# Optimization experiments

Hardware: AMD Instinct MI355X
Metric: run time of the kernel (lower is better)

The kernel has to match this reference:

```python
import jax, jax.numpy as jnp
import numpy as np

B = 131072
NF, E = 9, 8
D0 = NF * E  # 72
H = 64       # expert hidden
O = 8        # expert output
T, SE, SH = 3, 3, 3
VOCAB = 160000

PARAM_SHAPES = {
    "emb_table": (VOCAB, E),
    "spec0_W1": (T, SE, D0, H), "spec0_b1": (T, SE, H),
    "spec0_W2": (T, SE, H, O),  "spec0_b2": (T, SE, O),
    "shar0_W1": (SH, D0, H),    "shar0_b1": (SH, H),
    "shar0_W2": (SH, H, O),     "shar0_b2": (SH, O),
    "gate0_W1": (T, D0, H),     "gate0_b1": (T, H),
    "gate0_W2": (T, H, O),      "gate0_b2": (T, O),
    "gate0_W3": (T, O, SE + SH),
    "sgate0_W1": (D0, H), "sgate0_b1": (H,),
    "sgate0_W2": (H, O),  "sgate0_b2": (O,),
    "sgate0_W3": (O, T * SE + SH),
    "spec1_W1": (T, SE, O, H), "spec1_b1": (T, SE, H),
    "spec1_W2": (T, SE, H, O), "spec1_b2": (T, SE, O),
    "shar1_W1": (SH, O, H),    "shar1_b1": (SH, H),
    "shar1_W2": (SH, H, O),    "shar1_b2": (SH, O),
    "gate1_W1": (T, O, H),     "gate1_b1": (T, H),
    "gate1_W2": (T, H, O),     "gate1_b2": (T, O),
    "gate1_W3": (T, O, SE + SH),
    "tower_W": (T, O, 1), "tower_b": (T, 1),
}


def setup_inputs() -> dict:
    key = jax.random.key(0)
    keys = jax.random.split(key, len(PARAM_SHAPES) + 1)
    inp = {n: jax.random.normal(k, s, jnp.float32) * 0.1
           for (n, s), k in zip(PARAM_SHAPES.items(), keys[:-1])}
    inp["cat_idx"] = jax.random.randint(keys[-1], (B, NF), 0, VOCAB, jnp.int32)
    return inp


def _cgc(task_x, shared_x, sW1, sb1, sW2, sb2, hW1, hb1, hW2, hb2,
         gW1, gb1, gW2, gb2, gW3, sgate=None):
    """One CGC level. task_x: [T,B,in], shared_x: [B,in]."""
    # task-specific experts, batched over (task, expert)
    h = jax.nn.relu(jnp.einsum('tbi,teih->tebh', task_x, sW1) + sb1[:, :, None, :])
    spec = jax.nn.relu(jnp.einsum('tebh,teho->tebo', h, sW2) + sb2[:, :, None, :])  # [T,SE,B,O]
    # shared experts, batched over expert
    hs = jax.nn.relu(jnp.einsum('bi,eih->ebh', shared_x, hW1) + hb1[:, None, :])
    shar = jax.nn.relu(jnp.einsum('ebh,eho->ebo', hs, hW2) + hb2[:, None, :])       # [SH,B,O]
    # per-task gates: MLP[64,8] relu -> linear(no bias) -> softmax over SE+SH experts
    g = jax.nn.relu(jnp.einsum('tbi,tih->tbh', task_x, gW1) + gb1[:, None, :])
    g = jax.nn.relu(jnp.einsum('tbh,tho->tbo', g, gW2) + gb2[:, None, :])
    gw = jax.nn.softmax(jnp.einsum('tbo,toe->tbe', g, gW3), axis=-1)                # [T,B,SE+SH]
    experts = jnp.concatenate(
        [spec, jnp.broadcast_to(shar[None], (spec.shape[0],) + shar.shape)], axis=1)  # [T,SE+SH,B,O]
    task_out = jnp.einsum('tebo,tbe->tbo', experts, gw)                             # [T,B,O]
    if sgate is None:
        return task_out, None
    sgW1, sgb1, sgW2, sgb2, sgW3 = sgate
    gs = jax.nn.relu(shared_x @ sgW1 + sgb1)
    gs = jax.nn.relu(gs @ sgW2 + sgb2)
    gws = jax.nn.softmax(gs @ sgW3, axis=-1)                                        # [B,T*SE+SH]
    all_e = jnp.concatenate([spec.reshape(T * SE, spec.shape[2], O), shar], axis=0)  # [T*SE+SH,B,O]
    shared_out = jnp.einsum('ebo,be->bo', all_e, gws)
    return task_out, shared_out


def _forward(cat_idx, p):
    x = p["emb_table"][cat_idx].reshape(cat_idx.shape[0], -1)  # [B, 72]
    task_x = jnp.broadcast_to(x[None], (T,) + x.shape)
    task_x, shared_x = _cgc(
        task_x, x,
        p["spec0_W1"], p["spec0_b1"], p["spec0_W2"], p["spec0_b2"],
        p["shar0_W1"], p["shar0_b1"], p["shar0_W2"], p["shar0_b2"],
        p["gate0_W1"], p["gate0_b1"], p["gate0_W2"], p["gate0_b2"], p["gate0_W3"],
        sgate=(p["sgate0_W1"], p["sgate0_b1"], p["sgate0_W2"], p["sgate0_b2"], p["sgate0_W3"]))
    task_x, _ = _cgc(
        task_x, shared_x,
        p["spec1_W1"], p["spec1_b1"], p["spec1_W2"], p["spec1_b2"],
        p["shar1_W1"], p["shar1_b1"], p["shar1_W2"], p["shar1_b2"],
        p["gate1_W1"], p["gate1_b1"], p["gate1_W2"], p["gate1_b2"], p["gate1_W3"],
        sgate=None)
    # 3 sigmoid towers -> stacked [T, B, 1] (== dict task_0..task_2 in original)
    out = jax.nn.sigmoid(jnp.einsum('tbo,tok->tbk', task_x, p["tower_W"]) + p["tower_b"][:, None, :])
    return out


def reference(cat_idx, emb_table, spec0_W1, spec0_b1, spec0_W2, spec0_b2,
              shar0_W1, shar0_b1, shar0_W2, shar0_b2,
              gate0_W1, gate0_b1, gate0_W2, gate0_b2, gate0_W3,
              sgate0_W1, sgate0_b1, sgate0_W2, sgate0_b2, sgate0_W3,
              spec1_W1, spec1_b1, spec1_W2, spec1_b2,
              shar1_W1, shar1_b1, shar1_W2, shar1_b2,
              gate1_W1, gate1_b1, gate1_W2, gate1_b2, gate1_W3,
              tower_W, tower_b):
    p = dict(locals())
    p.pop('cat_idx')
    return _forward(cat_idx, p)
```

## Files before the change

### kernel.cpp

```cpp
#include <hip/hip_runtime.h>


#define NT 256
#define EPB 64

typedef unsigned short u16;
typedef unsigned int u32;
typedef __fp16 hv2 __attribute__((ext_vector_type(2)));
typedef __fp16 half8 __attribute__((ext_vector_type(8)));
typedef __attribute__((ext_vector_type(4))) float floatx4;

__device__ __forceinline__ u32 pkh2(float a, float b){
  hv2 v = __builtin_amdgcn_cvt_pkrtz(a, b);
  u32 r; __builtin_memcpy(&r, &v, 4); return r;
}
__device__ __forceinline__ u16 f2h(float a){
  __fp16 h = (__fp16)a; u16 r; __builtin_memcpy(&r, &h, 2); return r;
}
__device__ __forceinline__ float h2f(u16 v){
  __fp16 h; __builtin_memcpy(&h, &v, 2); return (float)h;
}
__device__ __forceinline__ float dot2(u32 a, u32 b, float c){
  hv2 av, bv; __builtin_memcpy(&av, &a, 4); __builtin_memcpy(&bv, &b, 4);
  return __builtin_amdgcn_fdot2(av, bv, c, false);
}

__device__ __forceinline__ int pi2(int s){
  return (s & 3)*16 + (s >> 2);
}

#define W1F0 0
#define W2F0 49152
#define W1F1 57344
#define W2F1 72704
#define OFF_b1P0 80384
#define OFF_b2P0 81408
#define OFF_b1P1 81664
#define OFF_b2P1 82624
#define OFF_G0W3 82864
#define OFF_SG0W3 83008
#define OFF_G1W3 83104
#define OFF_TW   83248
#define OFF_Tb   83272
#define CVT_TOTAL 83275

struct PSrc { const float* p[33]; };

__global__ void cvt_kernel(PSrc S, u32* __restrict__ wsU, float* __restrict__ wsF){
  int i = blockIdx.x*256 + threadIdx.x;
  if (i >= CVT_TOTAL) return;
  if (i < 49152){
    int j2 = i & 3, l = (i>>2)&63, tt = (i>>8)&3;
    int rest = i >> 10; int s = rest % 3, u = rest / 3;
    int k0 = s*32 + (l>>4)*8 + 2*j2;
    int h  = tt*16 + (l&15);
    const float* src = (u<9)  ? S.p[0]  + (u*72)*64
                     : (u<12) ? S.p[4]  + ((u-9)*72)*64
                     : (u<15) ? S.p[8]  + ((u-12)*72)*64
                              : S.p[13];
    float lo = (k0   < 72) ? src[(k0  )*64 + h] : 0.f;
    float hi = (k0+1 < 72) ? src[(k0+1)*64 + h] : 0.f;
    wsU[i] = pkh2(lo, hi);
    return;
  }
  i -= 49152;
  if (i < 8192){
    int j2 = i & 3, l = (i>>2)&63, ks = (i>>8)&1, u = i>>9;
    int s0 = ks*32 + (l>>4)*8 + 2*j2;
    int n = l & 15;
    const float* src = (u<9)  ? S.p[2]  + u*512
                     : (u<12) ? S.p[6]  + (u-9)*512
                     : (u<15) ? S.p[10] + (u-12)*512
                              : S.p[15];
    float lo = (n<8) ? src[pi2((s0  )&63)*8 + n] : 0.f;
    float hi = (n<8) ? src[pi2((s0+1)&63)*8 + n] : 0.f;
    wsU[W2F0 + i] = pkh2(lo, hi);
    return;
  }
  i -= 8192;
  if (i < 15360){
    int j2 = i & 3, l = (i>>2)&63, tt = (i>>8)&3, u = i>>10;
    int k0 = (l>>4)*8 + 2*j2;
    int n = tt*16 + (l&15);
    const float* src = (u<9) ? S.p[18] + (u*8)*64
                     : (u<12) ? S.p[22] + ((u-9)*8)*64
                              : S.p[26] + ((u-12)*8)*64;
    float lo = (k0   < 8) ? src[(k0  )*64 + n] : 0.f;
    float hi = (k0+1 < 8) ? src[(k0+1)*64 + n] : 0.f;
    wsU[W1F1 + i] = pkh2(lo, hi);
    return;
  }
  i -= 15360;
  if (i < 7680){
    int j2 = i & 3, l = (i>>2)&63, ks = (i>>8)&1, u = i>>9;
    int s0 = ks*32 + (l>>4)*8 + 2*j2;
    int n = l & 15;
    const float* src = (u<9) ? S.p[20] + u*512
                     : (u<12) ? S.p[24] + (u-9)*512
                              : S.p[28] + (u-12)*512;
    float lo = (n<8) ? src[pi2((s0  )&63)*8 + n] : 0.f;
    float hi = (n<8) ? src[pi2((s0+1)&63)*8 + n] : 0.f;
    wsU[W2F1 + i] = pkh2(lo, hi);
    return;
  }
  i -= 7680;
  if (i < 1024){
    int u = i>>6, r = i&63, c16 = r>>2, t = r&3;
    const float* src = (u<9) ? S.p[1]+u*64 : (u<12) ? S.p[5]+(u-9)*64
                     : (u<15) ? S.p[9]+(u-12)*64 : S.p[14];
    wsF[OFF_b1P0 + i] = src[t*16 + c16];
    return;
  }
  i -= 1024;
  if (i < 256){
    int u = i>>4, n = i&15;
    const float* src = (u<9) ? S.p[3]+u*8 : (u<12) ? S.p[7]+(u-9)*8
                     : (u<15) ? S.p[11]+(u-12)*8 : S.p[16];
    wsF[OFF_b2P0 + i] = (n<8) ? src[n] : 0.f;
    return;
  }
  i -= 256;
  if (i < 960){
    int u = i>>6, r = i&63, c16 = r>>2, t = r&3;
    const float* src = (u<9) ? S.p[19]+u*64 : (u<12) ? S.p[23]+(u-9)*64
                               : S.p[27]+(u-12)*64;
    wsF[OFF_b1P1 + i] = src[t*16 + c16];
    return;
  }
  i -= 960;
  if (i < 240){
    int u = i>>4, n = i&15;
    const float* src = (u<9) ? S.p[21]+u*8 : (u<12) ? S.p[25]+(u-9)*8
                               : S.p[29]+(u-12)*8;
    wsF[OFF_b2P1 + i] = (n<8) ? src[n] : 0.f;
    return;
  }
  i -= 240;
  if (i < 144){ wsF[OFF_G0W3 + i] = S.p[12][i]; return; }
  i -= 144;
  if (i < 96){ wsF[OFF_SG0W3 + i] = S.p[17][i]; return; }
  i -= 96;
  if (i < 144){ wsF[OFF_G1W3 + i] = S.p[30][i]; return; }
  i -= 144;
  if (i < 24){ wsF[OFF_TW + i] = S.p[31][i]; return; }
  i -= 24;
  wsF[OFF_Tb + i] = S.p[32][i];
}

template<int N>
__device__ __forceinline__ void softmaxT(float (&v)[N]){
  float m = v[0];
  #pragma unroll
  for (int i=1;i<N;i++) m = fmaxf(m, v[i]);
  float s = 0.f;
  #pragma unroll
  for (int i=0;i<N;i++){ v[i] = __expf(v[i]-m); s += v[i]; }
  float inv = 1.f/s;
  #pragma unroll
  for (int i=0;i<N;i++) v[i] *= inv;
}

__global__ __launch_bounds__(NT, 4) void ple_kernel(
    const float* __restrict__ emb, const int* __restrict__ cat,
    const u32* __restrict__ wsU, const float* __restrict__ P,
    float* __restrict__ out, int Btot)
{
  __shared__ u32 S_[9984];
  u32* xsA = S_;
  u32* obT = S_ + 3328;
  u32* hbW = S_ + 7680;
  const int tid = threadIdx.x;
  const int e = tid & 63;
  const int su = __builtin_amdgcn_readfirstlane(tid >> 6);
  const int lane = tid & 63;
  const int q = lane >> 4;
  const int c16 = lane & 15;
  const int shw_e = ((e>>2)&1)*4;

  {
    const int eg = blockIdx.x*EPB + e;
    auto ldf = [&](int f){
      int idx = cat[eg*9 + f];
      const float* ep = emb + (long)idx*8;
      float4 a = *(const float4*)ep;
      float4 b = *(const float4*)(ep+4);
      uint4 w; w.x = pkh2(a.x,a.y); w.y = pkh2(a.z,a.w);
      w.z = pkh2(b.x,b.y); w.w = pkh2(b.z,b.w);
      *(uint4*)(xsA + e*52 + f*4) = w;
    };
    ldf(su); ldf(su+4);
    if (su == 0) ldf(8);
    *(uint4*)(xsA + e*52 + 36 + su*4) = (uint4){0,0,0,0};
  }
  __syncthreads();

  u16* obp = (u16*)obT;
  const int sh16_q = ((q&1) ? 8 : 0);

  {
    u32* hbU = hbW + su*576;
    #pragma unroll 1
    for (int k4 = 0; k4 < 4; k4++){
      const int u = su*4 + k4;
      half8 bf[3][4];
      #pragma unroll
      for (int s=0;s<3;s++)
        #pragma unroll
        for (int t=0;t<4;t++)
          bf[s][t] = *(const half8*)(wsU + W1F0 + (((u*3+s)*4+t)*64 + lane)*4);
      float4 bias4 = *(const float4*)(P + OFF_b1P0 + u*64 + c16*4);
      float bias[4] = {bias4.x, bias4.y, bias4.z, bias4.w};
      const float ob2 = P[OFF_b2P0 + u*16 + c16];
      half8 w2f[2];
      #pragma unroll
      for (int ks=0;ks<2;ks++)
        w2f[ks] = *(const half8*)(wsU + W2F0 + ((u*2+ks)*64 + lane)*4);

      #pragma unroll 1
      for (int m=0;m<4;m++){
        half8 af[3];
        #pragma unroll
        for (int s=0;s<3;s++)
          af[s] = *(const half8*)(xsA + (m*16 + c16)*52 + s*16 + q*4);
        floatx4 acc[4];
        #pragma unroll
        for (int t=0;t<4;t++) acc[t] = (floatx4){bias[t],bias[t],bias[t],bias[t]};
        #pragma unroll
        for (int s=0;s<3;s++)
          #pragma unroll
          for (int t=0;t<4;t++)
            acc[t] = __builtin_amdgcn_mfma_f32_16x16x32_f16(af[s], bf[s][t], acc[t], 0,0,0);
        #pragma unroll
        for (int r=0;r<4;r++){
          uint2 hw;
          hw.x = pkh2(fmaxf(acc[0][r],0.f), fmaxf(acc[1][r],0.f));
          hw.y = pkh2(fmaxf(acc[2][r],0.f), fmaxf(acc[3][r],0.f));
          *(uint2*)(hbU + (q*4+r)*36 + 2*c16) = hw;
        }
        floatx4 oc = (floatx4){ob2, ob2, ob2, ob2};
        #pragma unroll
        for (int ks=0;ks<2;ks++){
          half8 haf = *(const half8*)(hbU + c16*36 + ks*16 + q*4);
          oc = __builtin_amdgcn_mfma_f32_16x16x32_f16(haf, w2f[ks], oc, 0,0,0);
        }
        if (c16 < 8){
          #pragma unroll
          for (int r=0;r<4;r++)
            obp[(m*16 + q*4 + r)*136 + sh16_q + c16*16 + u] = f2h(fmaxf(oc[r], 0.f));
        }
      }
    }
  }
  __syncthreads();

  u32* l1in = xsA;
  *(uint4*)(l1in + e*36 + 16 + su*4) = (uint4){0,0,0,0};
  {
    float wv[12];
    {
      const int ug = (su<3) ? 12+su : 15;
      float g8[8];
      #pragma unroll
      for (int j=0;j<8;j++) g8[j] = h2f(obp[e*136 + 2*shw_e + j*16 + ug]);
      if (su < 3){
        float lg[6];
        #pragma unroll
        for (int m=0;m<6;m++){
          float s = 0.f;
          #pragma unroll
          for (int j=0;j<8;j++) s = fmaf(g8[j], P[OFF_G0W3 + su*48 + j*6 + m], s);
          lg[m] = s;
        }
        softmaxT<6>(lg);
        #pragma unroll
        for (int k=0;k<12;k++)
          wv[k] = (k<9) ? (((k/3)==su) ? lg[k%3] : 0.f) : lg[k-6];
      } else {
        float lw[12];
        #pragma unroll
        for (int m=0;m<12;m++){
          float s = 0.f;
          #pragma unroll
          for (int j=0;j<8;j++) s = fmaf(g8[j], P[OFF_SG0W3 + j*12 + m], s);
          lw[m] = s;
        }
        softmaxT<12>(lw);
        #pragma unroll
        for (int k=0;k<12;k++) wv[k] = lw[k];
      }
    }
    u32 wp[6];
    #pragma unroll
    for (int p=0;p<6;p++) wp[p] = pkh2(wv[2*p], wv[2*p+1]);
    float in8[8];
    #pragma unroll
    for (int n=0;n<8;n++){
      const u32* rowp = obT + e*68 + shw_e + n*8;
      uint4 A = *(const uint4*)rowp;
      uint2 Bv = *(const uint2*)(rowp + 4);
      float s = dot2(A.x, wp[0], 0.f);
      s = dot2(A.y, wp[1], s);
      s = dot2(A.z, wp[2], s);
      s = dot2(A.w, wp[3], s);
      s = dot2(Bv.x, wp[4], s);
      s = dot2(Bv.y, wp[5], s);
      in8[n] = s;
    }
    const int dst = (su<3) ? su*4 : 12;
    uint4 lw4; lw4.x = pkh2(in8[0],in8[1]); lw4.y = pkh2(in8[2],in8[3]);
    lw4.z = pkh2(in8[4],in8[5]); lw4.w = pkh2(in8[6],in8[7]);
    *(uint4*)(l1in + e*36 + dst) = lw4;
  }
  __syncthreads();

  {
    u32* hbU = hbW + su*576;
    #pragma unroll 1
    for (int k4=0;k4<4;k4++){
      const int u = su*4 + k4;
      if (u >= 15) break;
      const int base_u = (u<9) ? (u/3)*4 : ((u<12) ? 12 : (u-12)*4);
      const int aoff = (q==0) ? base_u : (16 + q*4);
      half8 bf1[4];
      #pragma unroll
      for (int t=0;t<4;t++)
        bf1[t] = *(const half8*)(wsU + W1F1 + ((u*4+t)*64 + lane)*4);
      float4 bias4 = *(const float4*)(P + OFF_b1P1 + u*64 + c16*4);
      float bias[4] = {bias4.x, bias4.y, bias4.z, bias4.w};
      const float ob2 = P[OFF_b2P1 + u*16 + c16];
      half8 w2f[2];
      #pragma unroll
      for (int ks=0;ks<2;ks++)
        w2f[ks] = *(const half8*)(wsU + W2F1 + ((u*2+ks)*64 + lane)*4);

      #pragma unroll 1
      for (int m=0;m<4;m++){
        half8 af = *(const half8*)(l1in + (m*16 + c16)*36 + aoff);
        floatx4 acc[4];
        #pragma unroll
        for (int t=0;t<4;t++) acc[t] = (floatx4){bias[t],bias[t],bias[t],bias[t]};
        #pragma unroll
        for (int t=0;t<4;t++)
          acc[t] = __builtin_amdgcn_mfma_f32_16x16x32_f16(af, bf1[t], acc[t], 0,0,0);
        #pragma unroll
        for (int r=0;r<4;r++){
          uint2 hw;
          hw.x = pkh2(fmaxf(acc[0][r],0.f), fmaxf(acc[1][r],0.f));
          hw.y = pkh2(fmaxf(acc[2][r],0.f), fmaxf(acc[3][r],0.f));
          *(uint2*)(hbU + (q*4+r)*36 + 2*c16) = hw;
        }
        floatx4 oc = (floatx4){ob2, ob2, ob2, ob2};
        #pragma unroll
        for (int ks=0;ks<2;ks++){
          half8 haf = *(const half8*)(hbU + c16*36 + ks*16 + q*4);
          oc = __builtin_amdgcn_mfma_f32_16x16x32_f16(haf, w2f[ks], oc, 0,0,0);
        }
        if (c16 < 8){
          #pragma unroll
          for (int r=0;r<4;r++)
            obp[(m*16 + q*4 + r)*136 + sh16_q + c16*16 + u] = f2h(fmaxf(oc[r], 0.f));
        }
      }
    }
  }
  __syncthreads();

  if (su < 3){
    const int t = su;
    float g8[8];
    #pragma unroll
    for (int j=0;j<8;j++) g8[j] = h2f(obp[e*136 + 2*shw_e + j*16 + 12+t]);
    float lg[6];
    #pragma unroll
    for (int m=0;m<6;m++){
      float s = 0.f;
      #pragma unroll
      for (int j=0;j<8;j++) s = fmaf(g8[j], P[OFF_G1W3 + t*48 + j*6 + m], s);
      lg[m] = s;
    }
    softmaxT<6>(lg);
    float wv[12];
    #pragma unroll
    for (int k=0;k<12;k++)
      wv[k] = (k<9) ? (((k/3)==t) ? lg[k%3] : 0.f) : lg[k-6];
    u32 wp[6];
    #pragma unroll
    for (int p=0;p<6;p++) wp[p] = pkh2(wv[2*p], wv[2*p+1]);
    float s = P[OFF_Tb + t];
    #pragma unroll
    for (int n=0;n<8;n++){
      const u32* rowp = obT + e*68 + shw_e + n*8;
      uint4 A = *(const uint4*)rowp;
      uint2 Bv = *(const uint2*)(rowp + 4);
      float v = dot2(A.x, wp[0], 0.f);
      v = dot2(A.y, wp[1], v);
      v = dot2(A.z, wp[2], v);
      v = dot2(A.w, wp[3], v);
      v = dot2(Bv.x, wp[4], v);
      v = dot2(Bv.y, wp[5], v);
      s = fmaf(v, P[OFF_TW + t*8 + n], s);
    }
    out[t*Btot + blockIdx.x*EPB + e] = 1.f/(1.f + __expf(-s));
  }
}

extern "C" void kernel_launch(void* const* d_in, const int* in_sizes, int n_in,
                              void* d_out, int out_size, void* d_ws, size_t ws_size,
                              hipStream_t stream)
{
  const float* emb = (const float*)d_in[0];
  const int* cat = (const int*)d_in[34];
  float* out = (float*)d_out;
  u32* wsU = (u32*)d_ws;
  float* wsF = (float*)d_ws;
  PSrc S;
  for (int k=0;k<33;k++) S.p[k] = (const float*)d_in[k+1];
  const int B = in_sizes[34] / 9;

  cvt_kernel<<<(CVT_TOTAL+255)/256, 256, 0, stream>>>(S, wsU, wsF);
  ple_kernel<<<B/EPB, NT, 0, stream>>>(emb, cat, wsU, wsF, out, B);
}
```

Before: 189.4 us.

## Keep expert hidden activations in registers by transposing the first MFMA

The first expert matmul now swaps its A and B operands, so the output tile is transposed and each lane holds exactly the hidden values it needs as the A operand of the second MFMA. The hidden tile is packed to fp16 in registers instead of making a round trip through a per-wave LDS buffer. The W2 and bias weight preprocessing is re-permuted to match the new register layout. This removes the LDS stores and loads between the two MFMAs, shrinks shared memory, and raises launch bounds to 5 waves per SIMD, at the risk of register pressure or spills.

```diff
diff --git a/kernel.cpp b/kernel.cpp
--- a/kernel.cpp
+++ b/kernel.cpp
@@ -23,10 +23,6 @@
 __device__ __forceinline__ float dot2(u32 a, u32 b, float c){
   hv2 av, bv; __builtin_memcpy(&av, &a, 4); __builtin_memcpy(&bv, &b, 4);
   return __builtin_amdgcn_fdot2(av, bv, c, false);
-}
-
-__device__ __forceinline__ int pi2(int s){
-  return (s & 3)*16 + (s >> 2);
 }
 
 #define W1F0 0
@@ -66,14 +62,14 @@
   i -= 49152;
   if (i < 8192){
     int j2 = i & 3, l = (i>>2)&63, ks = (i>>8)&1, u = i>>9;
-    int s0 = ks*32 + (l>>4)*8 + 2*j2;
-    int n = l & 15;
+    int q = l >> 4, n = l & 15;
+    int h0 = (2*ks + ((2*j2)>>2))*16 + q*4 + ((2*j2)&3);
     const float* src = (u<9)  ? S.p[2]  + u*512
                      : (u<12) ? S.p[6]  + (u-9)*512
                      : (u<15) ? S.p[10] + (u-12)*512
                               : S.p[15];
-    float lo = (n<8) ? src[pi2((s0  )&63)*8 + n] : 0.f;
-    float hi = (n<8) ? src[pi2((s0+1)&63)*8 + n] : 0.f;
+    float lo = (n<8) ? src[h0*8 + n] : 0.f;
+    float hi = (n<8) ? src[(h0+1)*8 + n] : 0.f;
     wsU[W2F0 + i] = pkh2(lo, hi);
     return;
   }
@@ -93,22 +89,22 @@
   i -= 15360;
   if (i < 7680){
     int j2 = i & 3, l = (i>>2)&63, ks = (i>>8)&1, u = i>>9;
-    int s0 = ks*32 + (l>>4)*8 + 2*j2;
-    int n = l & 15;
+    int q = l >> 4, n = l & 15;
+    int h0 = (2*ks + ((2*j2)>>2))*16 + q*4 + ((2*j2)&3);
     const float* src = (u<9) ? S.p[20] + u*512
                      : (u<12) ? S.p[24] + (u-9)*512
                               : S.p[28] + (u-12)*512;
-    float lo = (n<8) ? src[pi2((s0  )&63)*8 + n] : 0.f;
-    float hi = (n<8) ? src[pi2((s0+1)&63)*8 + n] : 0.f;
+    float lo = (n<8) ? src[h0*8 + n] : 0.f;
+    float hi = (n<8) ? src[(h0+1)*8 + n] : 0.f;
     wsU[W2F1 + i] = pkh2(lo, hi);
     return;
   }
   i -= 7680;
   if (i < 1024){
-    int u = i>>6, r = i&63, c16 = r>>2, t = r&3;
+    int u = i>>6;
     const float* src = (u<9) ? S.p[1]+u*64 : (u<12) ? S.p[5]+(u-9)*64
                      : (u<15) ? S.p[9]+(u-12)*64 : S.p[14];
-    wsF[OFF_b1P0 + i] = src[t*16 + c16];
+    wsF[OFF_b1P0 + i] = src[i&63];
     return;
   }
   i -= 1024;
@@ -121,10 +117,10 @@
   }
   i -= 256;
   if (i < 960){
-    int u = i>>6, r = i&63, c16 = r>>2, t = r&3;
+    int u = i>>6;
     const float* src = (u<9) ? S.p[19]+u*64 : (u<12) ? S.p[23]+(u-9)*64
                                : S.p[27]+(u-12)*64;
-    wsF[OFF_b1P1 + i] = src[t*16 + c16];
+    wsF[OFF_b1P1 + i] = src[i&63];
     return;
   }
   i -= 960;
@@ -160,15 +156,14 @@
   for (int i=0;i<N;i++) v[i] *= inv;
 }
 
-__global__ __launch_bounds__(NT, 4) void ple_kernel(
+__global__ __launch_bounds__(NT, 5) void ple_kernel(
     const float* __restrict__ emb, const int* __restrict__ cat,
     const u32* __restrict__ wsU, const float* __restrict__ P,
     float* __restrict__ out, int Btot)
 {
-  __shared__ u32 S_[9984];
+  __shared__ u32 S_[7680];
   u32* xsA = S_;
   u32* obT = S_ + 3328;
-  u32* hbW = S_ + 7680;
   const int tid = threadIdx.x;
   const int e = tid & 63;
   const int su = __builtin_amdgcn_readfirstlane(tid >> 6);
@@ -198,7 +193,6 @@
   const int sh16_q = ((q&1) ? 8 : 0);
 
   {
-    u32* hbU = hbW + su*576;
     #pragma unroll 1
     for (int k4 = 0; k4 < 4; k4++){
       const int u = su*4 + k4;
@@ -208,8 +202,12 @@
         #pragma unroll
         for (int t=0;t<4;t++)
           bf[s][t] = *(const half8*)(wsU + W1F0 + (((u*3+s)*4+t)*64 + lane)*4);
-      float4 bias4 = *(const float4*)(P + OFF_b1P0 + u*64 + c16*4);
-      float bias[4] = {bias4.x, bias4.y, bias4.z, bias4.w};
+      floatx4 bias[4];
+      #pragma unroll
+      for (int t=0;t<4;t++){
+        float4 b4 = *(const float4*)(P + OFF_b1P0 + u*64 + t*16 + q*4);
+        bias[t] = (floatx4){b4.x, b4.y, b4.z, b4.w};
+      }
       const float ob2 = P[OFF_b2P0 + u*16 + c16];
       half8 w2f[2];
       #pragma unroll
@@ -224,23 +222,21 @@
           af[s] = *(const half8*)(xsA + (m*16 + c16)*52 + s*16 + q*4);
         floatx4 acc[4];
         #pragma unroll
-        for (int t=0;t<4;t++) acc[t] = (floatx4){bias[t],bias[t],bias[t],bias[t]};
+        for (int t=0;t<4;t++) acc[t] = bias[t];
         #pragma unroll
         for (int s=0;s<3;s++)
           #pragma unroll
           for (int t=0;t<4;t++)
-            acc[t] = __builtin_amdgcn_mfma_f32_16x16x32_f16(af[s], bf[s][t], acc[t], 0,0,0);
-        #pragma unroll
-        for (int r=0;r<4;r++){
-          uint2 hw;
-          hw.x = pkh2(fmaxf(acc[0][r],0.f), fmaxf(acc[1][r],0.f));
-          hw.y = pkh2(fmaxf(acc[2][r],0.f), fmaxf(acc[3][r],0.f));
-          *(uint2*)(hbU + (q*4+r)*36 + 2*c16) = hw;
-        }
+            acc[t] = __builtin_amdgcn_mfma_f32_16x16x32_f16(bf[s][t], af[s], acc[t], 0,0,0);
         floatx4 oc = (floatx4){ob2, ob2, ob2, ob2};
         #pragma unroll
         for (int ks=0;ks<2;ks++){
-          half8 haf = *(const half8*)(hbU + c16*36 + ks*16 + q*4);
+          u32 aw[4];
+          aw[0] = pkh2(fmaxf(acc[2*ks  ][0],0.f), fmaxf(acc[2*ks  ][1],0.f));
+          aw[1] = pkh2(fmaxf(acc[2*ks  ][2],0.f), fmaxf(acc[2*ks  ][3],0.f));
+          aw[2] = pkh2(fmaxf(acc[2*ks+1][0],0.f), fmaxf(acc[2*ks+1][1],0.f));
+          aw[3] = pkh2(fmaxf(acc[2*ks+1][2],0.f), fmaxf(acc[2*ks+1][3],0.f));
+          half8 haf; __builtin_memcpy(&haf, aw, 16);
           oc = __builtin_amdgcn_mfma_f32_16x16x32_f16(haf, w2f[ks], oc, 0,0,0);
         }
         if (c16 < 8){
@@ -314,7 +310,6 @@
   __syncthreads();
 
   {
-    u32* hbU = hbW + su*576;
     #pragma unroll 1
     for (int k4=0;k4<4;k4++){
       const int u = su*4 + k4;
@@ -325,8 +320,12 @@
       #pragma unroll
       for (int t=0;t<4;t++)
         bf1[t] = *(const half8*)(wsU + W1F1 + ((u*4+t)*64 + lane)*4);
-      float4 bias4 = *(const float4*)(P + OFF_b1P1 + u*64 + c16*4);
-      float bias[4] = {bias4.x, bias4.y, bias4.z, bias4.w};
+      floatx4 bias[4];
+      #pragma unroll
+      for (int t=0;t<4;t++){
+        float4 b4 = *(const float4*)(P + OFF_b1P1 + u*64 + t*16 + q*4);
+        bias[t] = (floatx4){b4.x, b4.y, b4.z, b4.w};
+      }
       const float ob2 = P[OFF_b2P1 + u*16 + c16];
       half8 w2f[2];
       #pragma unroll
@@ -338,21 +337,19 @@
         half8 af = *(const half8*)(l1in + (m*16 + c16)*36 + aoff);
         floatx4 acc[4];
         #pragma unroll
-        for (int t=0;t<4;t++) acc[t] = (floatx4){bias[t],bias[t],bias[t],bias[t]};
+        for (int t=0;t<4;t++) acc[t] = bias[t];
         #pragma unroll
         for (int t=0;t<4;t++)
-          acc[t] = __builtin_amdgcn_mfma_f32_16x16x32_f16(af, bf1[t], acc[t], 0,0,0);
-        #pragma unroll
-        for (int r=0;r<4;r++){
-          uint2 hw;
-          hw.x = pkh2(fmaxf(acc[0][r],0.f), fmaxf(acc[1][r],0.f));
-          hw.y = pkh2(fmaxf(acc[2][r],0.f), fmaxf(acc[3][r],0.f));
-          *(uint2*)(hbU + (q*4+r)*36 + 2*c16) = hw;
-        }
+          acc[t] = __builtin_amdgcn_mfma_f32_16x16x32_f16(bf1[t], af, acc[t], 0,0,0);
         floatx4 oc = (floatx4){ob2, ob2, ob2, ob2};
         #pragma unroll
         for (int ks=0;ks<2;ks++){
-          half8 haf = *(const half8*)(hbU + c16*36 + ks*16 + q*4);
+          u32 aw[4];
+          aw[0] = pkh2(fmaxf(acc[2*ks  ][0],0.f), fmaxf(acc[2*ks  ][1],0.f));
+          aw[1] = pkh2(fmaxf(acc[2*ks  ][2],0.f), fmaxf(acc[2*ks  ][3],0.f));
+          aw[2] = pkh2(fmaxf(acc[2*ks+1][0],0.f), fmaxf(acc[2*ks+1][1],0.f));
+          aw[3] = pkh2(fmaxf(acc[2*ks+1][2],0.f), fmaxf(acc[2*ks+1][3],0.f));
+          half8 haf; __builtin_memcpy(&haf, aw, 16);
           oc = __builtin_amdgcn_mfma_f32_16x16x32_f16(haf, w2f[ks], oc, 0,0,0);
         }
         if (c16 < 8){
```

Result: slower. 208.5 us (+10.1%).
